# Performance work log

Measured on AMD Instinct MI355X. Metric: run time of the kernel, lower is better.

Reference implementation:

```python
import jax, jax.numpy as jnp
import numpy as np

D_MODEL = 64
SEQ_LEN = 9
MAX_SL = 50
TIMESTAMP = 56
ACTION_NUM = 300
BATCH = 65536


def setup_inputs() -> dict:
    key = jax.random.key(0)
    ks = jax.random.split(key, 8)
    input_actions = jax.random.randint(ks[0], (BATCH, SEQ_LEN), 0, ACTION_NUM + 1)
    emb_table = jax.random.normal(ks[1], (ACTION_NUM + 1, D_MODEL), jnp.float32) * 0.02
    emb_table = emb_table.at[0].set(0.0)  # padding_idx=0
    M_w = jax.random.normal(ks[2], (MAX_SL, D_MODEL, D_MODEL), jnp.float32) * 0.05
    M_b = jax.random.normal(ks[3], (MAX_SL, D_MODEL), jnp.float32) * 0.05
    W_w = jax.random.normal(ks[4], (TIMESTAMP, D_MODEL, D_MODEL), jnp.float32) * 0.05
    W_b = jax.random.normal(ks[5], (TIMESTAMP, D_MODEL), jnp.float32) * 0.05
    out_w = jax.random.normal(ks[6], (ACTION_NUM, D_MODEL), jnp.float32) * 0.05
    out_b = jax.random.normal(ks[7], (ACTION_NUM,), jnp.float32) * 0.05
    return {"input_actions": input_actions, "emb_table": emb_table,
            "M_w": M_w, "M_b": M_b, "W_w": W_w, "W_b": W_b,
            "out_w": out_w, "out_b": out_b}


def reference(input_actions, emb_table, M_w, M_b, W_w, W_b, out_w, out_b):
    B, S = input_actions.shape
    d = emb_table.shape[1]
    ae = emb_table[input_actions]              # [B, S, d]
    ae_t = jnp.transpose(ae, (1, 0, 2))        # [S, B, d]
    # per-timestep weight selection, matching M[min(i, len(M)-1)] and W[i % timeStamp]
    m_idx = jnp.minimum(jnp.arange(S), M_w.shape[0] - 1)
    w_idx = jnp.arange(S) % W_w.shape[0]
    Mw, Mb = M_w[m_idx], M_b[m_idx]            # [S, d, d], [S, d]
    Ww, Wb = W_w[w_idx], W_b[w_idx]

    def step(hl, xs):
        x, mw, mb, ww, wb = xs
        # torch Linear: y = x @ W.T + b
        hl = jax.nn.sigmoid(x @ mw.T + mb + hl @ ww.T + wb)
        return hl, None

    hl0 = jnp.zeros((B, d), ae.dtype)
    hl, _ = jax.lax.scan(step, hl0, (ae_t, Mw, Mb, Ww, Wb))
    return hl @ out_w.T + out_b               # [B, actionNum]
```

## Files before the change

kernel.cpp:

```cpp
#include <hip/hip_runtime.h>
#include <hip/hip_bf16.h>


#define SEQ     9
#define DMODEL  64
#define ANUM    300

#define WS_MW   0
#define WS_OW   73728
#define WS_EMB  94208
#define WS_END  113472
#define WS_BSUM_BYTES (WS_END * 2)

#define BSOFF   61440
#define HSOFF   62592
#define SLTOT   78976

typedef __attribute__((ext_vector_type(8))) short  bf16x8;
typedef __attribute__((ext_vector_type(4))) float  f32x4;

#define MFMA __builtin_amdgcn_mfma_f32_16x16x32_bf16

__device__ __forceinline__ unsigned short f2b(float f) {
    union { float f; unsigned int u; } x; x.f = f;
    unsigned int r = x.u + 0x7FFFu + ((x.u >> 16) & 1u);
    return (unsigned short)(r >> 16);
}

__device__ __forceinline__ float sigmoid_fast(float v) {
    return __builtin_amdgcn_rcpf(1.f + __expf(-v));
}

__device__ __forceinline__ void async16(const unsigned short* g, unsigned short* l) {
    __builtin_amdgcn_global_load_lds(
        (const __attribute__((address_space(1))) unsigned int*)g,
        (__attribute__((address_space(3))) unsigned int*)l, 16, 0, 0);
}

#define PP_TOTAL (73728 + 20480 + 19264 + 576)

__global__ void prepack(const float* __restrict__ Mw, const float* __restrict__ Ww,
                        const float* __restrict__ outw, const float* __restrict__ emb,
                        const float* __restrict__ Mb, const float* __restrict__ Wb,
                        unsigned short* __restrict__ wsb, float* __restrict__ bsum)
{
    int t = blockIdx.x * 256 + threadIdx.x;
    if (t < 73728) {
        int s    = t >> 13;
        int r    = t & 8191;
        int kind = r >> 12;
        int f    = r & 4095;
        int nt   = f >> 10;
        int kb   = (f >> 9) & 1;
        int lane = (f >> 3) & 63;
        int j    = f & 7;
        int nr   = nt * 16 + (lane & 15);
        int k    = kb * 32 + ((lane >> 4) << 3) + j;
        const float* src = kind ? Ww : Mw;
        wsb[WS_MW + t] = f2b(src[(s * DMODEL + nr) * DMODEL + k]);
        return;
    }
    t -= 73728;
    if (t < 20480) {
        int j    = t & 7;
        int lane = (t >> 3) & 63;
        int kb   = (t >> 9) & 1;
        int nt   = (t >> 10) & 3;
        int cc   = t >> 12;
        int col  = cc * 64 + nt * 16 + (lane & 15);
        int k    = kb * 32 + ((lane >> 4) << 3) + j;
        float v  = (col < ANUM) ? outw[col * DMODEL + k] : 0.f;
        wsb[WS_OW + t] = f2b(v);
        return;
    }
    t -= 20480;
    if (t < 19264) { wsb[WS_EMB + t] = f2b(emb[t]); return; }
    t -= 19264;
    if (t < 576)   { bsum[t] = Mb[t] + Wb[t]; }
}

__global__ __launch_bounds__(1024, 4)
void carnn_main(const int* __restrict__ acts,
                const unsigned short* __restrict__ wsb,
                const float* __restrict__ bsum,
                const float* __restrict__ outb,
                float* __restrict__ out)
{
    __shared__ __align__(16) unsigned short SL[SLTOT];

    const int tid  = threadIdx.x;
    const int lane = tid & 63;
    const int wv   = tid >> 6;
    const int lrow = lane & 15;
    const int quad = lane >> 4;

    const int brow = (blockIdx.x * 16 + wv) * 16 + lrow;
    const int rowS = brow * SEQ;

    for (int c = wv; c < 120; c += 16) {
        const int goff = (c < 8) ? (c * 512) : ((c + 8) * 512);
        async16(wsb + WS_MW + goff + lane * 8, &SL[c * 512]);
    }
    {
        const unsigned short* bs = (const unsigned short*)bsum;
        if (wv == 13) async16(bs + lane * 8,         &SL[BSOFF]);
        if (wv == 14) async16(bs + 512 + lane * 8,   &SL[BSOFF + 512]);
        if (wv == 15 && lane < 16)
                      async16(bs + 1024 + lane * 8,  &SL[BSOFF + 1024]);
    }

    const unsigned short* Eb = wsb + WS_EMB;
    int idc = acts[rowS];
    bf16x8 xc0 = *(const bf16x8*)(Eb + idc * DMODEL + quad * 8);
    bf16x8 xc1 = *(const bf16x8*)(Eb + idc * DMODEL + 32 + quad * 8);
    int idn = acts[rowS + 1];

    char* const SB = (char*)SL;
    const int swz    = (lrow & 7) << 4;
    const int hbyte  = HSOFF * 2 + wv * 2048 + lrow * 128;
    const int rbyte0 = hbyte + ((quad * 16) ^ swz);
    const int rbyte1 = hbyte + ((64 + quad * 16) ^ swz);

    __syncthreads();

    const float* BSf = (const float*)&SL[BSOFF];

    #pragma unroll
    for (int s = 0; s < SEQ; ++s) {
        bf16x8 xn0, xn1;
        if (s + 1 < SEQ) {
            xn0 = *(const bf16x8*)(Eb + idn * DMODEL + quad * 8);
            xn1 = *(const bf16x8*)(Eb + idn * DMODEL + 32 + quad * 8);
            if (s + 2 < SEQ) idn = acts[rowS + s + 2];
        }
        bf16x8 h0, h1;
        if (s > 0) {
            h0 = *(const bf16x8*)(SB + rbyte0);
            h1 = *(const bf16x8*)(SB + rbyte1);
        }
        const unsigned short* WB;
        if (s == 0)     WB = &SL[0];
        else if (s < 8) WB = &SL[4096 + (s - 1) * 8192];
        else            WB = wsb + WS_MW + 8 * 8192;

        #pragma unroll
        for (int nt = 0; nt < 4; ++nt) {
            const unsigned short* Mf = WB + nt * 1024 + lane * 8;
            bf16x8 am0 = *(const bf16x8*)Mf;
            bf16x8 am1 = *(const bf16x8*)(Mf + 512);
            f32x4 acc = *(const f32x4*)(BSf + s * 64 + nt * 16 + quad * 4);
            acc = MFMA(am0, xc0, acc, 0, 0, 0);
            acc = MFMA(am1, xc1, acc, 0, 0, 0);
            if (s > 0) {
                const unsigned short* Wf = WB + 4096 + nt * 1024 + lane * 8;
                bf16x8 aw0 = *(const bf16x8*)Wf;
                bf16x8 aw1 = *(const bf16x8*)(Wf + 512);
                acc = MFMA(aw0, h0, acc, 0, 0, 0);
                acc = MFMA(aw1, h1, acc, 0, 0, 0);
            }
            unsigned int u0 = (unsigned int)f2b(sigmoid_fast(acc[0]))
                            | ((unsigned int)f2b(sigmoid_fast(acc[1])) << 16);
            unsigned int u1 = (unsigned int)f2b(sigmoid_fast(acc[2]))
                            | ((unsigned int)f2b(sigmoid_fast(acc[3])) << 16);
            *(uint2*)(SB + hbyte + ((nt * 32 + quad * 8) ^ swz)) = make_uint2(u0, u1);
        }
        if (s + 1 < SEQ) { xc0 = xn0; xc1 = xn1; }
    }

    bf16x8 h0 = *(const bf16x8*)(SB + rbyte0);
    bf16x8 h1 = *(const bf16x8*)(SB + rbyte1);

    __syncthreads();
    for (int c = wv; c < 40; c += 16)
        async16(wsb + WS_OW + c * 512 + lane * 8, &SL[c * 512]);
    {
        const unsigned short* ob = (const unsigned short*)outb;
        if (wv == 12)               async16(ob + lane * 8,       &SL[BSOFF]);
        if (wv == 13 && lane < 11)  async16(ob + 512 + lane * 8, &SL[BSOFF + 512]);
    }
    __syncthreads();

    const float* OBf = (const float*)&SL[BSOFF];
    float* orow = out + brow * ANUM;

    #pragma unroll
    for (int t = 0; t < 19; ++t) {
        const int cc = t >> 2, nt = t & 3;
        const unsigned short* Of = &SL[cc * 4096 + nt * 1024 + lane * 8];
        bf16x8 a0 = *(const bf16x8*)Of;
        bf16x8 a1 = *(const bf16x8*)(Of + 512);
        const int col0 = cc * 64 + nt * 16 + quad * 4;

        f32x4 acc;
        if (col0 < ANUM) acc = *(const f32x4*)(OBf + col0);
        else             acc = (f32x4){0.f, 0.f, 0.f, 0.f};
        acc = MFMA(a0, h0, acc, 0, 0, 0);
        acc = MFMA(a1, h1, acc, 0, 0, 0);

        if (col0 < ANUM)
            *(f32x4*)(orow + col0) = acc;
    }
}

extern "C" void kernel_launch(void* const* d_in, const int* in_sizes, int n_in,
                              void* d_out, int out_size, void* d_ws, size_t ws_size,
                              hipStream_t stream) {
    const int*   acts = (const int*)  d_in[0];
    const float* emb  = (const float*)d_in[1];
    const float* Mw   = (const float*)d_in[2];
    const float* Mb   = (const float*)d_in[3];
    const float* Ww   = (const float*)d_in[4];
    const float* Wb   = (const float*)d_in[5];
    const float* outw = (const float*)d_in[6];
    const float* outb = (const float*)d_in[7];
    float* out = (float*)d_out;
    (void)in_sizes; (void)n_in; (void)ws_size; (void)out_size;

    unsigned short* wsb = (unsigned short*)d_ws;
    float* bsum = (float*)((char*)d_ws + WS_BSUM_BYTES);

    prepack<<<(PP_TOTAL + 255) / 256, 256, 0, stream>>>(Mw, Ww, outw, emb, Mb, Wb, wsb, bsum);
    carnn_main<<<65536 / 256, 1024, 0, stream>>>(acts, wsb, bsum, outb, out);
}
```

Baseline: 119.4 us.

## Software-pipeline input projection one step ahead of recurrent MFMA chain

Computes the input-side projection (M weights times embedding plus bias) for step s+1 after the hidden-state update of step s. The recurrent critical path then only carries the two W·h MFMAs per tile plus the sigmoid. Embedding prefetch moves two steps ahead. This takes the input MFMAs and their LDS loads off the serial dependency chain so they can overlap with the latency of h reads and writes. In exchange the kernel holds more registers for the extra accumulators and prefetched embeddings, which may hurt occupancy under 1024-thread launch bounds.

```diff
diff --git a/kernel.cpp b/kernel.cpp
--- a/kernel.cpp
+++ b/kernel.cpp
@@ -110,10 +110,13 @@
     }
 
     const unsigned short* Eb = wsb + WS_EMB;
-    int idc = acts[rowS];
-    bf16x8 xc0 = *(const bf16x8*)(Eb + idc * DMODEL + quad * 8);
-    bf16x8 xc1 = *(const bf16x8*)(Eb + idc * DMODEL + 32 + quad * 8);
-    int idn = acts[rowS + 1];
+    int id0  = acts[rowS];
+    int id1  = acts[rowS + 1];
+    int idn2 = acts[rowS + 2];
+    bf16x8 xc0 = *(const bf16x8*)(Eb + id0 * DMODEL + quad * 8);
+    bf16x8 xc1 = *(const bf16x8*)(Eb + id0 * DMODEL + 32 + quad * 8);
+    bf16x8 xn0 = *(const bf16x8*)(Eb + id1 * DMODEL + quad * 8);
+    bf16x8 xn1 = *(const bf16x8*)(Eb + id1 * DMODEL + 32 + quad * 8);
 
     char* const SB = (char*)SL;
     const int swz    = (lrow & 7) << 4;
@@ -125,34 +128,40 @@
 
     const float* BSf = (const float*)&SL[BSOFF];
 
+    f32x4 xacc[4];
+    #pragma unroll
+    for (int nt = 0; nt < 4; ++nt) {
+        const unsigned short* Mf = &SL[nt * 1024 + lane * 8];
+        bf16x8 am0 = *(const bf16x8*)Mf;
+        bf16x8 am1 = *(const bf16x8*)(Mf + 512);
+        f32x4 a = *(const f32x4*)(BSf + nt * 16 + quad * 4);
+        a = MFMA(am0, xc0, a, 0, 0, 0);
+        a = MFMA(am1, xc1, a, 0, 0, 0);
+        xacc[nt] = a;
+    }
+
     #pragma unroll
     for (int s = 0; s < SEQ; ++s) {
-        bf16x8 xn0, xn1;
-        if (s + 1 < SEQ) {
-            xn0 = *(const bf16x8*)(Eb + idn * DMODEL + quad * 8);
-            xn1 = *(const bf16x8*)(Eb + idn * DMODEL + 32 + quad * 8);
-            if (s + 2 < SEQ) idn = acts[rowS + s + 2];
-        }
+        bf16x8 xm0, xm1;
+        if (s + 2 < SEQ) {
+            xm0 = *(const bf16x8*)(Eb + idn2 * DMODEL + quad * 8);
+            xm1 = *(const bf16x8*)(Eb + idn2 * DMODEL + 32 + quad * 8);
+            if (s + 3 < SEQ) idn2 = acts[rowS + s + 3];
+        }
+
         bf16x8 h0, h1;
         if (s > 0) {
             h0 = *(const bf16x8*)(SB + rbyte0);
             h1 = *(const bf16x8*)(SB + rbyte1);
         }
-        const unsigned short* WB;
-        if (s == 0)     WB = &SL[0];
-        else if (s < 8) WB = &SL[4096 + (s - 1) * 8192];
-        else            WB = wsb + WS_MW + 8 * 8192;
-
+        const unsigned short* WBh = (s == 0) ? (const unsigned short*)nullptr
+                                  : (s < 8)  ? &SL[4096 + (s - 1) * 8192 + 4096]
+                                             : wsb + WS_MW + 8 * 8192 + 4096;
         #pragma unroll
         for (int nt = 0; nt < 4; ++nt) {
-            const unsigned short* Mf = WB + nt * 1024 + lane * 8;
-            bf16x8 am0 = *(const bf16x8*)Mf;
-            bf16x8 am1 = *(const bf16x8*)(Mf + 512);
-            f32x4 acc = *(const f32x4*)(BSf + s * 64 + nt * 16 + quad * 4);
-            acc = MFMA(am0, xc0, acc, 0, 0, 0);
-            acc = MFMA(am1, xc1, acc, 0, 0, 0);
+            f32x4 acc = xacc[nt];
             if (s > 0) {
-                const unsigned short* Wf = WB + 4096 + nt * 1024 + lane * 8;
+                const unsigned short* Wf = WBh + nt * 1024 + lane * 8;
                 bf16x8 aw0 = *(const bf16x8*)Wf;
                 bf16x8 aw1 = *(const bf16x8*)(Wf + 512);
                 acc = MFMA(aw0, h0, acc, 0, 0, 0);
@@ -164,7 +173,23 @@
                             | ((unsigned int)f2b(sigmoid_fast(acc[3])) << 16);
             *(uint2*)(SB + hbyte + ((nt * 32 + quad * 8) ^ swz)) = make_uint2(u0, u1);
         }
-        if (s + 1 < SEQ) { xc0 = xn0; xc1 = xn1; }
+        asm volatile("" ::: "memory");
+
+        if (s + 1 < SEQ) {
+            const unsigned short* WBm = (s + 1 < 8) ? &SL[4096 + s * 8192]
+                                                    : wsb + WS_MW + 8 * 8192;
+            #pragma unroll
+            for (int nt = 0; nt < 4; ++nt) {
+                const unsigned short* Mf = WBm + nt * 1024 + lane * 8;
+                bf16x8 am0 = *(const bf16x8*)Mf;
+                bf16x8 am1 = *(const bf16x8*)(Mf + 512);
+                f32x4 a = *(const f32x4*)(BSf + (s + 1) * 64 + nt * 16 + quad * 4);
+                a = MFMA(am0, xn0, a, 0, 0, 0);
+                a = MFMA(am1, xn1, a, 0, 0, 0);
+                xacc[nt] = a;
+            }
+            if (s + 2 < SEQ) { xn0 = xm0; xn1 = xm1; }
+        }
     }
 
     bf16x8 h0 = *(const bf16x8*)(SB + rbyte0);
```

New measurement: 119.9 us. About the same (+0.5%).
